# Performance work log

Hardware: AMD Instinct MI355X
Metric: run time of the kernel (lower is better)

The kernel has to match this reference:

```python
import jax, jax.numpy as jnp
import numpy as np

T, D_IN, D_OUT, E = 8192, 1024, 1024, 8
LN_EPS = 1e-5


def setup_inputs() -> dict:
    key = jax.random.key(0)
    k1, k2, k3 = jax.random.split(key, 3)
    x = jax.random.normal(k1, (T, D_IN), dtype=jnp.float32)
    # tokens are pre-sorted by expert; equal load => capacity = T // E per expert
    expert_frequency = jnp.full((E,), T // E, dtype=jnp.int64)
    # per-expert Linear(input_dim, output_dim) params
    W = jax.random.normal(k2, (E, D_IN, D_OUT), dtype=jnp.float32) / np.sqrt(D_IN)
    b = jax.random.normal(k3, (E, D_OUT), dtype=jnp.float32) * 0.02
    # per-expert LayerNorm(output_dim) affine params
    ln_gamma = jnp.ones((E, D_OUT), dtype=jnp.float32)
    ln_beta = jnp.zeros((E, D_OUT), dtype=jnp.float32)
    return {
        "expert_ordered_input": x,
        "expert_frequency": expert_frequency,
        "W": W,
        "b": b,
        "ln_gamma": ln_gamma,
        "ln_beta": ln_beta,
    }


def reference(expert_ordered_input, expert_frequency, W, b, ln_gamma, ln_beta):
    # Grouped-GEMM form of: split tokens by expert_frequency, apply per-expert
    # LayerBlock (Linear -> relu -> LayerNorm), then concat along token dim.
    # Frequencies are equal (capacity = T // E), so the ragged split is a reshape.
    x = expert_ordered_input
    n_tok, d_in = x.shape
    n_exp = W.shape[0]
    cap = n_tok // n_exp  # static capacity per expert
    xe = x.reshape(n_exp, cap, d_in)                       # [E, cap, d_in]
    h = jnp.einsum("ecd,edf->ecf", xe, W) + b[:, None, :]  # [E, cap, d_out]
    h = jax.nn.relu(h)
    mu = jnp.mean(h, axis=-1, keepdims=True)
    var = jnp.var(h, axis=-1, keepdims=True)
    hn = (h - mu) * jax.lax.rsqrt(var + LN_EPS)
    out = hn * ln_gamma[:, None, :] + ln_beta[:, None, :]
    return out.reshape(n_tok, -1)                          # concat over experts
```

## Files before the change

kernel.cpp:

```cpp
#include <hip/hip_runtime.h>
#include <hip/hip_bf16.h>
#include <stdint.h>

#define T_TOK 8192
#define DIN   1024
#define DOUT  1024
#define NEXP  8
#define CAP   1024
#define LN_EPS 1e-5f

#define BM 128
#define BN 128
#define BK 32
#define LDSS 48

typedef __attribute__((ext_vector_type(8))) short short8;
typedef __attribute__((ext_vector_type(4))) float f32x4;

__device__ __forceinline__ unsigned short f2bf(float f) {
    union { float f; unsigned int u; } v; v.f = f;
    unsigned int u = v.u;
    unsigned int r = u + 0x7FFFu + ((u >> 16) & 1u);
    return (unsigned short)(r >> 16);
}

__global__ __launch_bounds__(256) void wt_kernel(const float* __restrict__ W,
                                                 unsigned short* __restrict__ Wt) {
    __shared__ float tile[32][33];
    int e  = blockIdx.z;
    int k0 = blockIdx.y * 32;
    int n0 = blockIdx.x * 32;
    const float* Wp = W + (size_t)e * DIN * DOUT;
    unsigned short* Wtp = Wt + (size_t)e * DIN * DOUT;
    int tx = threadIdx.x;
    int ty = threadIdx.y;
#pragma unroll
    for (int r = 0; r < 4; r++)
        tile[ty + r * 8][tx] = Wp[(size_t)(k0 + ty + r * 8) * DOUT + (n0 + tx)];
    __syncthreads();
#pragma unroll
    for (int r = 0; r < 4; r++)
        Wtp[(size_t)(n0 + ty + r * 8) * DIN + (k0 + tx)] = f2bf(tile[tx][ty + r * 8]);
}

__global__ __launch_bounds__(256, 2) void gemm_kernel(
    const float* __restrict__ X,
    const unsigned short* __restrict__ Wt,
    const float* __restrict__ Bias,
    float* __restrict__ H)
{
    __shared__ unsigned short As[BM * LDSS];
    __shared__ unsigned short Bs[BN * LDSS];

    int blk = blockIdx.x;
    int e   = blk >> 6;
    int tt  = blk & 63;
    int m0  = (tt >> 3) * BM;
    int n0  = (tt & 7) * BN;

    int tid  = threadIdx.x;
    int wave = tid >> 6;
    int lane = tid & 63;
    int wm   = (wave >> 1) * 64;
    int wn   = (wave & 1) * 64;
    int lrow = lane & 15;
    int quad = lane >> 4;

    const float* Xe = X + (size_t)(e * CAP + m0) * DIN;
    const unsigned short* We = Wt + (size_t)e * DOUT * DIN + (size_t)n0 * DIN;

    f32x4 acc[4][4];
#pragma unroll
    for (int i = 0; i < 4; i++)
#pragma unroll
        for (int j = 0; j < 4; j++)
            acc[i][j] = (f32x4)(0.0f);

    for (int k0 = 0; k0 < DIN; k0 += BK) {
#pragma unroll
        for (int i = 0; i < 4; i++) {
            int idx = tid + i * 256;
            int row = idx >> 3;
            int c4  = idx & 7;
            const float4 xv = *(const float4*)(Xe + (size_t)row * DIN + k0 + c4 * 4);
            ushort4 bv;
            bv.x = f2bf(xv.x); bv.y = f2bf(xv.y); bv.z = f2bf(xv.z); bv.w = f2bf(xv.w);
            *(ushort4*)&As[row * LDSS + c4 * 4] = bv;
        }
#pragma unroll
        for (int i = 0; i < 2; i++) {
            int idx = tid + i * 256;
            int row = idx >> 2;
            int c   = idx & 3;
            uint4 wv = *(const uint4*)(We + (size_t)row * DIN + k0 + c * 8);
            *(uint4*)&Bs[row * LDSS + c * 8] = wv;
        }
        __syncthreads();

        short8 af[4], bf[4];
#pragma unroll
        for (int i = 0; i < 4; i++)
            af[i] = *(const short8*)&As[(wm + i * 16 + lrow) * LDSS + quad * 8];
#pragma unroll
        for (int j = 0; j < 4; j++)
            bf[j] = *(const short8*)&Bs[(wn + j * 16 + lrow) * LDSS + quad * 8];
#pragma unroll
        for (int i = 0; i < 4; i++)
#pragma unroll
            for (int j = 0; j < 4; j++)
                acc[i][j] = __builtin_amdgcn_mfma_f32_16x16x32_bf16(af[i], bf[j], acc[i][j], 0, 0, 0);
        __syncthreads();
    }

    float bias[4];
#pragma unroll
    for (int j = 0; j < 4; j++)
        bias[j] = Bias[e * DOUT + n0 + wn + j * 16 + lrow];

    int tok0 = e * CAP + m0 + wm;
#pragma unroll
    for (int i = 0; i < 4; i++) {
#pragma unroll
        for (int j = 0; j < 4; j++) {
            int col = n0 + wn + j * 16 + lrow;
#pragma unroll
            for (int r = 0; r < 4; r++) {
                int row = tok0 + i * 16 + quad * 4 + r;
                float v = acc[i][j][r] + bias[j];
                v = fmaxf(v, 0.0f);
                H[(size_t)row * DOUT + col] = v;
            }
        }
    }
}

__global__ __launch_bounds__(256) void ln_kernel(float* __restrict__ H,
                                                 const float* __restrict__ G,
                                                 const float* __restrict__ Bt) {
    int row = blockIdx.x;
    int e   = row >> 10;
    int tid  = threadIdx.x;
    int wave = tid >> 6;
    int lane = tid & 63;
    float* hp = H + (size_t)row * DOUT;

    float4 x = *(const float4*)(hp + tid * 4);
    float s  = x.x + x.y + x.z + x.w;
    float ss = fmaf(x.x, x.x, fmaf(x.y, x.y, fmaf(x.z, x.z, x.w * x.w)));

#pragma unroll
    for (int m = 32; m >= 1; m >>= 1) {
        s  += __shfl_xor(s, m);
        ss += __shfl_xor(ss, m);
    }
    __shared__ float red[8];
    if (lane == 0) { red[wave] = s; red[4 + wave] = ss; }
    __syncthreads();
    float ts  = red[0] + red[1] + red[2] + red[3];
    float tss = red[4] + red[5] + red[6] + red[7];

    float mean = ts * (1.0f / DOUT);
    float var  = tss * (1.0f / DOUT) - mean * mean;
    var = fmaxf(var, 0.0f);
    float rs = rsqrtf(var + LN_EPS);

    float4 g = *(const float4*)(G  + (size_t)e * DOUT + tid * 4);
    float4 b = *(const float4*)(Bt + (size_t)e * DOUT + tid * 4);
    float4 y;
    y.x = (x.x - mean) * rs * g.x + b.x;
    y.y = (x.y - mean) * rs * g.y + b.y;
    y.z = (x.z - mean) * rs * g.z + b.z;
    y.w = (x.w - mean) * rs * g.w + b.w;
    *(float4*)(hp + tid * 4) = y;
}

extern "C" void kernel_launch(void* const* d_in, const int* in_sizes, int n_in,
                              void* d_out, int out_size, void* d_ws, size_t ws_size,
                              hipStream_t stream) {
    const float* x  = (const float*)d_in[0];
    const float* W  = (const float*)d_in[2];
    const float* b  = (const float*)d_in[3];
    const float* g  = (const float*)d_in[4];
    const float* be = (const float*)d_in[5];
    unsigned short* Wt = (unsigned short*)d_ws;
    float* out = (float*)d_out;

    dim3 tb(32, 8);
    dim3 tg(32, 32, 8);
    wt_kernel<<<tg, tb, 0, stream>>>(W, Wt);
    gemm_kernel<<<dim3(512), dim3(256), 0, stream>>>(x, Wt, b, out);
    ln_kernel<<<dim3(8192), dim3(256), 0, stream>>>(out, g, be);
}
```

Baseline: 163.4 us.

## Pre-convert X to bf16 and stage GEMM tiles via direct global-to-LDS loads

Adds a separate pass that converts X to bf16 in workspace, so the GEMM streams half the bytes and can use global_load_lds to copy 16-byte chunks straight into unpadded LDS tiles. The block mapping changes to put experts in the low bits, and the W transpose kernel switches to float4 loads and ushort4 stores. The cost is an extra kernel plus a full round trip of X through memory, and the unpadded LDS layout may cause bank conflicts. A fallback path keeps the old GEMM when the workspace is too small.

```diff
diff --git a/kernel.cpp b/kernel.cpp
--- a/kernel.cpp
+++ b/kernel.cpp
@@ -22,6 +22,22 @@
     unsigned int u = v.u;
     unsigned int r = u + 0x7FFFu + ((u >> 16) & 1u);
     return (unsigned short)(r >> 16);
+}
+
+__device__ __forceinline__ void gld16(void* l, const void* g) {
+    __builtin_amdgcn_global_load_lds(
+        (const __attribute__((address_space(1))) unsigned int*)(uintptr_t)g,
+        (__attribute__((address_space(3))) unsigned int*)(uintptr_t)l,
+        16, 0, 0);
+}
+
+__global__ __launch_bounds__(256) void xb_kernel(const float* __restrict__ X,
+                                                 unsigned short* __restrict__ Xb) {
+    int i = blockIdx.x * 256 + threadIdx.x;
+    float4 v = ((const float4*)X)[i];
+    ushort4 o;
+    o.x = f2bf(v.x); o.y = f2bf(v.y); o.z = f2bf(v.z); o.w = f2bf(v.w);
+    ((ushort4*)Xb)[i] = o;
 }
 
 __global__ __launch_bounds__(256) void wt_kernel(const float* __restrict__ W,
@@ -32,18 +48,108 @@
     int n0 = blockIdx.x * 32;
     const float* Wp = W + (size_t)e * DIN * DOUT;
     unsigned short* Wtp = Wt + (size_t)e * DIN * DOUT;
-    int tx = threadIdx.x;
-    int ty = threadIdx.y;
-#pragma unroll
-    for (int r = 0; r < 4; r++)
-        tile[ty + r * 8][tx] = Wp[(size_t)(k0 + ty + r * 8) * DOUT + (n0 + tx)];
+    int tid = threadIdx.x;
+    {
+        int k  = tid >> 3;
+        int c4 = tid & 7;
+        float4 v = *(const float4*)(Wp + (size_t)(k0 + k) * DOUT + n0 + c4 * 4);
+        tile[k][c4 * 4 + 0] = v.x; tile[k][c4 * 4 + 1] = v.y;
+        tile[k][c4 * 4 + 2] = v.z; tile[k][c4 * 4 + 3] = v.w;
+    }
     __syncthreads();
-#pragma unroll
-    for (int r = 0; r < 4; r++)
-        Wtp[(size_t)(n0 + ty + r * 8) * DIN + (k0 + tx)] = f2bf(tile[tx][ty + r * 8]);
-}
-
-__global__ __launch_bounds__(256, 2) void gemm_kernel(
+    {
+        int n  = tid >> 3;
+        int kc = tid & 7;
+        ushort4 o;
+        o.x = f2bf(tile[kc * 4 + 0][n]);
+        o.y = f2bf(tile[kc * 4 + 1][n]);
+        o.z = f2bf(tile[kc * 4 + 2][n]);
+        o.w = f2bf(tile[kc * 4 + 3][n]);
+        *(ushort4*)(Wtp + (size_t)(n0 + n) * DIN + k0 + kc * 4) = o;
+    }
+}
+
+__global__ __launch_bounds__(256) void gemm2_kernel(
+    const unsigned short* __restrict__ Xb,
+    const unsigned short* __restrict__ Wt,
+    const float* __restrict__ Bias,
+    float* __restrict__ H)
+{
+    __shared__ unsigned short As[BM * BK];
+    __shared__ unsigned short Bs[BN * BK];
+
+    int blk = blockIdx.x;
+    int e   = blk & 7;
+    int m0  = (blk >> 6) * BM;
+    int n0  = ((blk >> 3) & 7) * BN;
+
+    int tid  = threadIdx.x;
+    int wave = tid >> 6;
+    int lane = tid & 63;
+    int wm   = (wave >> 1) * 64;
+    int wn   = (wave & 1) * 64;
+    int lrow = lane & 15;
+    int quad = lane >> 4;
+
+    const unsigned short* Ag = Xb + (size_t)(e * CAP + m0) * DIN;
+    const unsigned short* Bg = Wt + (size_t)e * DOUT * DIN + (size_t)n0 * DIN;
+
+    int l0 = tid;
+    int l1 = tid + 256;
+    int ar0 = l0 >> 2, ac0 = (l0 & 3) * 8;
+    int ar1 = l1 >> 2, ac1 = (l1 & 3) * 8;
+
+    f32x4 acc[4][4];
+#pragma unroll
+    for (int i = 0; i < 4; i++)
+#pragma unroll
+        for (int j = 0; j < 4; j++)
+            acc[i][j] = (f32x4)(0.0f);
+
+    for (int k0 = 0; k0 < DIN; k0 += BK) {
+        gld16(&As[l0 * 8], Ag + (size_t)ar0 * DIN + k0 + ac0);
+        gld16(&As[l1 * 8], Ag + (size_t)ar1 * DIN + k0 + ac1);
+        gld16(&Bs[l0 * 8], Bg + (size_t)ar0 * DIN + k0 + ac0);
+        gld16(&Bs[l1 * 8], Bg + (size_t)ar1 * DIN + k0 + ac1);
+        __syncthreads();
+
+        short8 af[4], bf[4];
+#pragma unroll
+        for (int i = 0; i < 4; i++)
+            af[i] = *(const short8*)&As[(wm + i * 16 + lrow) * BK + quad * 8];
+#pragma unroll
+        for (int j = 0; j < 4; j++)
+            bf[j] = *(const short8*)&Bs[(wn + j * 16 + lrow) * BK + quad * 8];
+#pragma unroll
+        for (int i = 0; i < 4; i++)
+#pragma unroll
+            for (int j = 0; j < 4; j++)
+                acc[i][j] = __builtin_amdgcn_mfma_f32_16x16x32_bf16(af[i], bf[j], acc[i][j], 0, 0, 0);
+        __syncthreads();
+    }
+
+    float bias[4];
+#pragma unroll
+    for (int j = 0; j < 4; j++)
+        bias[j] = Bias[e * DOUT + n0 + wn + j * 16 + lrow];
+
+    int tok0 = e * CAP + m0 + wm;
+#pragma unroll
+    for (int i = 0; i < 4; i++) {
+#pragma unroll
+        for (int j = 0; j < 4; j++) {
+            int col = n0 + wn + j * 16 + lrow;
+#pragma unroll
+            for (int r = 0; r < 4; r++) {
+                int row = tok0 + i * 16 + quad * 4 + r;
+                float v = acc[i][j][r] + bias[j];
+                H[(size_t)row * DOUT + col] = fmaxf(v, 0.0f);
+            }
+        }
+    }
+}
+
+__global__ __launch_bounds__(256, 2) void gemm_fb_kernel(
     const float* __restrict__ X,
     const unsigned short* __restrict__ Wt,
     const float* __restrict__ Bias,
@@ -51,13 +157,11 @@
 {
     __shared__ unsigned short As[BM * LDSS];
     __shared__ unsigned short Bs[BN * LDSS];
-
     int blk = blockIdx.x;
     int e   = blk >> 6;
     int tt  = blk & 63;
     int m0  = (tt >> 3) * BM;
     int n0  = (tt & 7) * BN;
-
     int tid  = threadIdx.x;
     int wave = tid >> 6;
     int lane = tid & 63;
@@ -65,17 +169,14 @@
     int wn   = (wave & 1) * 64;
     int lrow = lane & 15;
     int quad = lane >> 4;
-
     const float* Xe = X + (size_t)(e * CAP + m0) * DIN;
     const unsigned short* We = Wt + (size_t)e * DOUT * DIN + (size_t)n0 * DIN;
-
     f32x4 acc[4][4];
 #pragma unroll
     for (int i = 0; i < 4; i++)
 #pragma unroll
         for (int j = 0; j < 4; j++)
             acc[i][j] = (f32x4)(0.0f);
-
     for (int k0 = 0; k0 < DIN; k0 += BK) {
 #pragma unroll
         for (int i = 0; i < 4; i++) {
@@ -96,7 +197,6 @@
             *(uint4*)&Bs[row * LDSS + c * 8] = wv;
         }
         __syncthreads();
-
         short8 af[4], bf[4];
 #pragma unroll
         for (int i = 0; i < 4; i++)
@@ -111,15 +211,13 @@
                 acc[i][j] = __builtin_amdgcn_mfma_f32_16x16x32_bf16(af[i], bf[j], acc[i][j], 0, 0, 0);
         __syncthreads();
     }
-
     float bias[4];
 #pragma unroll
     for (int j = 0; j < 4; j++)
         bias[j] = Bias[e * DOUT + n0 + wn + j * 16 + lrow];
-
     int tok0 = e * CAP + m0 + wm;
 #pragma unroll
-    for (int i = 0; i < 4; i++) {
+    for (int i = 0; i < 4; i++)
 #pragma unroll
         for (int j = 0; j < 4; j++) {
             int col = n0 + wn + j * 16 + lrow;
@@ -127,11 +225,9 @@
             for (int r = 0; r < 4; r++) {
                 int row = tok0 + i * 16 + quad * 4 + r;
                 float v = acc[i][j][r] + bias[j];
-                v = fmaxf(v, 0.0f);
-                H[(size_t)row * DOUT + col] = v;
+                H[(size_t)row * DOUT + col] = fmaxf(v, 0.0f);
             }
         }
-    }
 }
 
 __global__ __launch_bounds__(256) void ln_kernel(float* __restrict__ H,
@@ -147,7 +243,6 @@
     float4 x = *(const float4*)(hp + tid * 4);
     float s  = x.x + x.y + x.z + x.w;
     float ss = fmaf(x.x, x.x, fmaf(x.y, x.y, fmaf(x.z, x.z, x.w * x.w)));
-
 #pragma unroll
     for (int m = 32; m >= 1; m >>= 1) {
         s  += __shfl_xor(s, m);
@@ -158,12 +253,9 @@
     __syncthreads();
     float ts  = red[0] + red[1] + red[2] + red[3];
     float tss = red[4] + red[5] + red[6] + red[7];
-
     float mean = ts * (1.0f / DOUT);
-    float var  = tss * (1.0f / DOUT) - mean * mean;
-    var = fmaxf(var, 0.0f);
+    float var  = fmaxf(tss * (1.0f / DOUT) - mean * mean, 0.0f);
     float rs = rsqrtf(var + LN_EPS);
-
     float4 g = *(const float4*)(G  + (size_t)e * DOUT + tid * 4);
     float4 b = *(const float4*)(Bt + (size_t)e * DOUT + tid * 4);
     float4 y;
@@ -182,12 +274,21 @@
     const float* b  = (const float*)d_in[3];
     const float* g  = (const float*)d_in[4];
     const float* be = (const float*)d_in[5];
+    float* out = (float*)d_out;
+
     unsigned short* Wt = (unsigned short*)d_ws;
-    float* out = (float*)d_out;
-
-    dim3 tb(32, 8);
-    dim3 tg(32, 32, 8);
-    wt_kernel<<<tg, tb, 0, stream>>>(W, Wt);
-    gemm_kernel<<<dim3(512), dim3(256), 0, stream>>>(x, Wt, b, out);
-    ln_kernel<<<dim3(8192), dim3(256), 0, stream>>>(out, g, be);
-}
+    const size_t WT_BYTES = (size_t)NEXP * DIN * DOUT * 2;
+    const size_t XB_BYTES = (size_t)T_TOK * DIN * 2;
+
+    dim3 tb(256);
+    wt_kernel<<<dim3(32, 32, 8), tb, 0, stream>>>(W, Wt);
+
+    if (ws_size >= WT_BYTES + XB_BYTES) {
+        unsigned short* Xb = (unsigned short*)((char*)d_ws + WT_BYTES);
+        xb_kernel<<<dim3(8192), tb, 0, stream>>>(x, Xb);
+        gemm2_kernel<<<dim3(512), tb, 0, stream>>>(Xb, Wt, b, out);
+    } else {
+        gemm_fb_kernel<<<dim3(512), tb, 0, stream>>>(x, Wt, b, out);
+    }
+    ln_kernel<<<dim3(8192), tb, 0, stream>>>(out, g, be);
+}
```

After: 153.0 us. 1.07x faster.
